# Kernel optimization log

Hardware: AMD Instinct MI355X
Metric: run time of the kernel (lower is better)

## Reference

```python
import jax, jax.numpy as jnp
import numpy as np


def setup_inputs() -> dict:
    key = jax.random.key(0)
    k1, k2 = jax.random.split(key)
    B, S, D = 8, 4096, 1024
    E, P = 8, 4
    x = jax.random.normal(k1, (B, S, D), dtype=jnp.float32)
    phi_kernel = jax.random.normal(k2, (D, E * P), dtype=jnp.float32) * (1.0 / np.sqrt(D))
    phi_bias = jnp.zeros((E * P,), dtype=jnp.float32)
    return {"x": x, "phi_kernel": phi_kernel, "phi_bias": phi_bias,
            "num_experts": E, "num_slots": P}


def reference(x, phi_kernel, phi_bias, num_experts, num_slots):
    B, S, D = x.shape
    E, P = num_experts, num_slots
    # phi logits: [B,S,E,P]
    phi_logits = (jnp.einsum('bsd,dk->bsk', x, phi_kernel) + phi_bias).reshape(B, S, E, P)
    # softmax over the sequence axis (each slot is a convex combo of tokens)
    phi_weights = jax.nn.softmax(phi_logits, axis=1)
    # soft slots: weighted sum over tokens -> [B,E,P,D] (fused, no [B,S,E,P,D] blowup)
    soft_slots = jnp.einsum('bsd,bsep->bepd', x, phi_weights)
    expert_inputs = soft_slots.reshape(B, E, P * D)
    expert_weights = jnp.full((B, S, E), 1.0 / E, dtype=x.dtype)
    expert_indices = jnp.broadcast_to(jnp.arange(E, dtype=jnp.int32)[None, None, :], (B, S, E))
    return (expert_weights, expert_indices, phi_weights, soft_slots, expert_inputs)
```

## Files before the change

kernel.cpp:

```cpp
#include <hip/hip_runtime.h>
#include <hip/hip_bf16.h>

#define B 8
#define S 4096
#define DD 1024
#define KK 32

typedef __attribute__((ext_vector_type(8))) short bf16x8;
typedef __attribute__((ext_vector_type(16))) float f32x16;
typedef __attribute__((ext_vector_type(4))) unsigned int u32x4;

static __device__ __forceinline__ unsigned short f2bf(float f) {
    unsigned int u = __builtin_bit_cast(unsigned int, f);
    u += 0x7FFFu + ((u >> 16) & 1u);
    return (unsigned short)(u >> 16);
}
static __device__ __forceinline__ unsigned int pkbf(float a, float b) {
    return (unsigned int)f2bf(a) | ((unsigned int)f2bf(b) << 16);
}
static __device__ __forceinline__ float bf2f(unsigned int u16) {
    return __builtin_bit_cast(float, u16 << 16);
}

__global__ __launch_bounds__(256) void k0_phit(const float* __restrict__ phi,
                                               unsigned short* __restrict__ phiT) {
    __shared__ float lt[32][33];
    const int d0 = blockIdx.x * 32;
    const int tid = threadIdx.x;
#pragma unroll
    for (int i = 0; i < 4; ++i) {
        int slot = tid + i * 256;
        int d = slot >> 5, k = slot & 31;
        lt[d][k] = phi[(size_t)(d0 + d) * KK + k];
    }
    __syncthreads();
    const int k = tid >> 3, c = tid & 7, d = c * 4;
    short4 pk;
    pk.x = (short)f2bf(lt[d + 0][k]);
    pk.y = (short)f2bf(lt[d + 1][k]);
    pk.z = (short)f2bf(lt[d + 2][k]);
    pk.w = (short)f2bf(lt[d + 3][k]);
    *(short4*)(phiT + (size_t)k * DD + d0 + d) = pk;
}

__global__ __launch_bounds__(256) void k1_logits(const float* __restrict__ x,
                                                 const unsigned short* __restrict__ phiT,
                                                 const float* __restrict__ bias,
                                                 unsigned short* __restrict__ lpb) {
    __shared__ float lt[4][32 * 33];

    const int tid = threadIdx.x;
    const int wv = __builtin_amdgcn_readfirstlane(tid >> 6);
    const int lane = tid & 63;
    const int l31 = lane & 31;
    const int half = lane >> 5;

    const int gw = blockIdx.x * 4 + wv;
    const int dq = gw & 3;
    const int stile = (gw >> 2) & 127;
    const int b = gw >> 9;
    const int s0 = stile * 32;

    const float* xr = x + ((size_t)(b * S + s0 + l31)) * DD + dq * 256 + half * 8;
    const unsigned short* pr = phiT + (size_t)l31 * DD + dq * 256 + half * 8;

    f32x16 acc;
    {
        float bv = (dq == 0) ? bias[l31] : 0.f;
#pragma unroll
        for (int r = 0; r < 16; ++r) acc[r] = bv;
    }

    float4 a0[2], a1[2];
    bf16x8 bf[2];
    auto ld = [&](int ks, int slot) {
        a0[slot] = *(const float4*)(xr + ks * 16);
        a1[slot] = *(const float4*)(xr + ks * 16 + 4);
        bf[slot] = *(const bf16x8*)(pr + ks * 16);
    };

    ld(0, 0);
    ld(1, 1);
#pragma unroll
    for (int ks = 0; ks < 16; ++ks) {
        const int cur = ks & 1;
        u32x4 t;
        t[0] = pkbf(a0[cur].x, a0[cur].y);
        t[1] = pkbf(a0[cur].z, a0[cur].w);
        t[2] = pkbf(a1[cur].x, a1[cur].y);
        t[3] = pkbf(a1[cur].z, a1[cur].w);
        bf16x8 af = __builtin_bit_cast(bf16x8, t);
        bf16x8 bc = bf[cur];
        if (ks < 14) ld(ks + 2, cur);
        acc = __builtin_amdgcn_mfma_f32_32x32x16_bf16(af, bc, acc, 0, 0, 0);
    }

    float* mylt = lt[wv];
#pragma unroll
    for (int r = 0; r < 16; ++r) {
        int row = (r & 3) + 8 * (r >> 2) + 4 * half;
        mylt[l31 * 33 + row] = acc[r];
    }
    {
        const int sb = half * 16;
        unsigned int w[8];
#pragma unroll
        for (int i = 0; i < 8; ++i)
            w[i] = pkbf(mylt[l31 * 33 + sb + 2 * i], mylt[l31 * 33 + sb + 2 * i + 1]);
        unsigned short* o = lpb + (((size_t)dq * B + b) * KK + l31) * S + s0 + sb;
        *(uint4*)o = make_uint4(w[0], w[1], w[2], w[3]);
        *(uint4*)(o + 8) = make_uint4(w[4], w[5], w[6], w[7]);
    }
}

__global__ __launch_bounds__(256) void k2_expsum(const unsigned short* __restrict__ lpb,
                                                 unsigned short* __restrict__ eT,
                                                 float* __restrict__ psum2) {
    const int bid = blockIdx.x;
    const int h = bid & 1;
    const int k = (bid >> 1) & 31;
    const int b = bid >> 6;
    const int tid = threadIdx.x;
    const int wave = tid >> 6, lane = tid & 63;

    const uint4* lp4 = (const uint4*)lpb;
    const size_t row4 = ((size_t)b * KK + k) * (S / 8) + h * 256 + tid;

    uint4 p0 = lp4[row4];
    uint4 p1 = lp4[(size_t)1 * (B * KK * S / 8) + row4];
    uint4 p2 = lp4[(size_t)2 * (B * KK * S / 8) + row4];
    uint4 p3 = lp4[(size_t)3 * (B * KK * S / 8) + row4];

    const unsigned int* q0 = &p0.x;
    const unsigned int* q1 = &p1.x;
    const unsigned int* q2 = &p2.x;
    const unsigned int* q3 = &p3.x;

    float e[8];
    float lsum = 0.f;
#pragma unroll
    for (int i = 0; i < 4; ++i) {
        float vlo = bf2f(q0[i] & 0xFFFFu) + bf2f(q1[i] & 0xFFFFu)
                  + bf2f(q2[i] & 0xFFFFu) + bf2f(q3[i] & 0xFFFFu);
        float vhi = bf2f(q0[i] >> 16) + bf2f(q1[i] >> 16)
                  + bf2f(q2[i] >> 16) + bf2f(q3[i] >> 16);
        e[2 * i] = __expf(vlo);
        e[2 * i + 1] = __expf(vhi);
        lsum += e[2 * i] + e[2 * i + 1];
    }
    uint4 o;
    o.x = pkbf(e[0], e[1]);
    o.y = pkbf(e[2], e[3]);
    o.z = pkbf(e[4], e[5]);
    o.w = pkbf(e[6], e[7]);
    ((uint4*)eT)[row4] = o;

#pragma unroll
    for (int off = 32; off >= 1; off >>= 1) lsum += __shfl_xor(lsum, off, 64);
    __shared__ float red[4];
    if (lane == 0) red[wave] = lsum;
    __syncthreads();
    if (tid == 0) psum2[(b * KK + k) * 2 + h] = red[0] + red[1] + red[2] + red[3];
}

__global__ __launch_bounds__(256) void k2b_linv(const float* __restrict__ psum2,
                                                float* __restrict__ Linv) {
    const int t = threadIdx.x;
    Linv[t] = 1.0f / (psum2[2 * t] + psum2[2 * t + 1]);
}

__global__ __launch_bounds__(256) void k2d_pw(const unsigned short* __restrict__ eT,
                                              const float* __restrict__ Linv,
                                              float* __restrict__ pw_out) {
    __shared__ float tile[128][33];
    const int b = blockIdx.x >> 5;
    const int sc = blockIdx.x & 31;
    const int s0 = sc * 128;
    const int tid = threadIdx.x;

    const int k = tid >> 3, part = tid & 7;
    const float scale = Linv[b * KK + k];
    const unsigned short* er = eT + ((size_t)b * KK + k) * S + s0 + part * 16;
    uint4 r0 = *(const uint4*)er;
    uint4 r1 = *(const uint4*)(er + 8);
    const unsigned int* q0 = &r0.x;
    const unsigned int* q1 = &r1.x;
#pragma unroll
    for (int i = 0; i < 4; ++i) {
        tile[part * 16 + 2 * i][k]     = bf2f(q0[i] & 0xFFFFu) * scale;
        tile[part * 16 + 2 * i + 1][k] = bf2f(q0[i] >> 16) * scale;
        tile[part * 16 + 8 + 2 * i][k]     = bf2f(q1[i] & 0xFFFFu) * scale;
        tile[part * 16 + 8 + 2 * i + 1][k] = bf2f(q1[i] >> 16) * scale;
    }
    __syncthreads();

    float* ob = pw_out + ((size_t)b * S + s0) * KK;
#pragma unroll
    for (int i = 0; i < 4; ++i) {
        const int idx4 = tid + i * 256;
        const int sl = idx4 >> 3, kq = idx4 & 7;
        float4 v4 = make_float4(tile[sl][kq * 4 + 0], tile[sl][kq * 4 + 1],
                                tile[sl][kq * 4 + 2], tile[sl][kq * 4 + 3]);
        ((float4*)ob)[idx4] = v4;
    }
}

__global__ __launch_bounds__(256) void k3_slots(const float* __restrict__ x,
                                                const unsigned short* __restrict__ eT,
                                                float* __restrict__ part) {
    const int tid = threadIdx.x;
    const int wv = __builtin_amdgcn_readfirstlane(tid >> 6);
    const int lane = tid & 63;
    const int l31 = lane & 31;
    const int half = lane >> 5;

    const int gw = blockIdx.x * 4 + wv;
    const int sc = gw & 7;
    const int dt = (gw >> 3) & 31;
    const int b = gw >> 8;

    const unsigned short* ar = eT + ((size_t)b * KK + l31) * S + sc * 512 + half * 8;
    const float* xc = x + ((size_t)(b * S + sc * 512 + half * 8)) * DD + dt * 32 + l31;

    f32x16 acc;
#pragma unroll
    for (int r = 0; r < 16; ++r) acc[r] = 0.f;

    float xb[2][8];
    bf16x8 ab[2];
    auto ld = [&](int ks, int slot) {
#pragma unroll
        for (int j = 0; j < 8; ++j)
            xb[slot][j] = xc[(size_t)(ks * 16 + j) * DD];
        ab[slot] = *(const bf16x8*)(ar + ks * 16);
    };

    ld(0, 0);
    ld(1, 1);
#pragma unroll 8
    for (int ks = 0; ks < 32; ++ks) {
        const int cur = ks & 1;
        u32x4 t;
        t[0] = pkbf(xb[cur][0], xb[cur][1]);
        t[1] = pkbf(xb[cur][2], xb[cur][3]);
        t[2] = pkbf(xb[cur][4], xb[cur][5]);
        t[3] = pkbf(xb[cur][6], xb[cur][7]);
        bf16x8 bfr = __builtin_bit_cast(bf16x8, t);
        bf16x8 ac = ab[cur];
        if (ks < 30) ld(ks + 2, cur);
        acc = __builtin_amdgcn_mfma_f32_32x32x16_bf16(ac, bfr, acc, 0, 0, 0);
    }

    float* pp = part + (((size_t)sc * B + b) * KK) * DD + dt * 32 + l31;
#pragma unroll
    for (int r = 0; r < 16; ++r) {
        int kmoe = (r & 3) + 8 * (r >> 2) + 4 * half;
        pp[(size_t)kmoe * DD] = acc[r];
    }
}

__global__ __launch_bounds__(256) void k4_finalize(const float* __restrict__ part,
                                                   const float* __restrict__ Linv,
                                                   float* __restrict__ out) {
    const int idx = blockIdx.x * 256 + threadIdx.x;
    const float4* p4 = (const float4*)part;

    float4 sv = p4[idx];
#pragma unroll
    for (int c = 1; c < 8; ++c) {
        float4 t = p4[(size_t)c * 65536 + idx];
        sv.x += t.x; sv.y += t.y; sv.z += t.z; sv.w += t.w;
    }
    const int f = idx * 4;
    const float scale = Linv[(f >> 15) * KK + ((f >> 10) & 31)];
    sv.x *= scale; sv.y *= scale; sv.z *= scale; sv.w *= scale;

    ((float4*)(out + 1572864))[idx] = sv;
    ((float4*)(out + 1835008))[idx] = sv;
    ((float4*)out)[idx] = make_float4(0.125f, 0.125f, 0.125f, 0.125f);
    float base = (float)(f & 7);
    ((float4*)(out + 262144))[idx] = make_float4(base, base + 1.f, base + 2.f, base + 3.f);
}

extern "C" void kernel_launch(void* const* d_in, const int* in_sizes, int n_in,
                              void* d_out, int out_size, void* d_ws, size_t ws_size,
                              hipStream_t stream) {
    const float* x    = (const float*)d_in[0];
    const float* phi  = (const float*)d_in[1];
    const float* bias = (const float*)d_in[2];
    float* out = (float*)d_out;

    float* ws = (float*)d_ws;
    unsigned short* lpb  = (unsigned short*)ws;
    unsigned short* eT   = (unsigned short*)(ws + 2097152);
    float* psum2 = ws + 2621440;
    float* Linv  = ws + 2621952;
    unsigned short* phiT = (unsigned short*)(ws + 2622208);
    float* part  = ws + 2638592;
    float* pw_out = out + 524288;

    k0_phit<<<dim3(32), dim3(256), 0, stream>>>(phi, phiT);
    k1_logits<<<dim3(1024), dim3(256), 0, stream>>>(x, phiT, bias, lpb);
    k2_expsum<<<dim3(512), dim3(256), 0, stream>>>(lpb, eT, psum2);
    k2b_linv<<<dim3(1), dim3(256), 0, stream>>>(psum2, Linv);
    k2d_pw<<<dim3(256), dim3(256), 0, stream>>>(eT, Linv, pw_out);
    k3_slots<<<dim3(512), dim3(256), 0, stream>>>(x, eT, part);
    k4_finalize<<<dim3(256), dim3(256), 0, stream>>>(part, Linv, out);
}
```

Baseline: 245.8 us.

## Fuse all stages into one cooperative persistent kernel with grid syncs

```diff
diff --git a/kernel.cpp b/kernel.cpp
--- a/kernel.cpp
+++ b/kernel.cpp
@@ -1,5 +1,8 @@
 #include <hip/hip_runtime.h>
 #include <hip/hip_bf16.h>
+#include <hip/hip_cooperative_groups.h>
+
+namespace cg = cooperative_groups;
 
 #define B 8
 #define S 4096
@@ -18,8 +21,223 @@
 static __device__ __forceinline__ unsigned int pkbf(float a, float b) {
     return (unsigned int)f2bf(a) | ((unsigned int)f2bf(b) << 16);
 }
+static __device__ __forceinline__ unsigned int pkbf_t(float lo, float hi) {
+    return __builtin_amdgcn_perm(__builtin_bit_cast(unsigned int, hi),
+                                 __builtin_bit_cast(unsigned int, lo),
+                                 0x07060302u);
+}
 static __device__ __forceinline__ float bf2f(unsigned int u16) {
     return __builtin_bit_cast(float, u16 << 16);
+}
+
+__global__ __launch_bounds__(256, 4) void fused_all(const float* __restrict__ x,
+                                                    const float* __restrict__ phi,
+                                                    const float* __restrict__ bias,
+                                                    float* __restrict__ ws,
+                                                    float* __restrict__ out) {
+    __shared__ __align__(16) char smraw[16896];
+    __shared__ float sLinv[256];
+    __shared__ float sred[4];
+
+    unsigned short* lpb = (unsigned short*)ws;
+    unsigned short* eT  = (unsigned short*)(ws + 2097152);
+    float* psum4 = ws + 2621440;
+    float* part  = ws + 2622464;
+    float* pw_out = out + 524288;
+
+    cg::grid_group grid = cg::this_grid();
+
+    const int bid = blockIdx.x;
+    const int tid = threadIdx.x;
+    const int wv = __builtin_amdgcn_readfirstlane(tid >> 6);
+    const int lane = tid & 63;
+    const int l31 = lane & 31;
+    const int half = lane >> 5;
+    const int nb = gridDim.x;
+
+    for (int gw = bid * 4 + wv; gw < 4096; gw += nb * 4) {
+        const int dq = gw & 3;
+        const int stile = (gw >> 2) & 127;
+        const int b = gw >> 9;
+        const int s0 = stile * 32;
+
+        const float* xr = x + ((size_t)(b * S + s0 + l31)) * DD + dq * 256 + half * 8;
+        const float* pcol = phi + (size_t)(dq * 256 + half * 8) * KK + l31;
+
+        f32x16 acc;
+        {
+            float bv = (dq == 0) ? bias[l31] : 0.f;
+#pragma unroll
+            for (int r = 0; r < 16; ++r) acc[r] = bv;
+        }
+
+        float4 a0[2], a1[2];
+        float pq[2][8];
+        auto ld = [&](int ks, int slot) {
+            a0[slot] = *(const float4*)(xr + ks * 16);
+            a1[slot] = *(const float4*)(xr + ks * 16 + 4);
+#pragma unroll
+            for (int j = 0; j < 8; ++j)
+                pq[slot][j] = pcol[(size_t)(ks * 16 + j) * KK];
+        };
+
+        ld(0, 0);
+        ld(1, 1);
+#pragma unroll
+        for (int ks = 0; ks < 16; ++ks) {
+            const int cur = ks & 1;
+            u32x4 ta, tb;
+            ta[0] = pkbf_t(a0[cur].x, a0[cur].y);
+            ta[1] = pkbf_t(a0[cur].z, a0[cur].w);
+            ta[2] = pkbf_t(a1[cur].x, a1[cur].y);
+            ta[3] = pkbf_t(a1[cur].z, a1[cur].w);
+            tb[0] = pkbf_t(pq[cur][0], pq[cur][1]);
+            tb[1] = pkbf_t(pq[cur][2], pq[cur][3]);
+            tb[2] = pkbf_t(pq[cur][4], pq[cur][5]);
+            tb[3] = pkbf_t(pq[cur][6], pq[cur][7]);
+            bf16x8 af = __builtin_bit_cast(bf16x8, ta);
+            bf16x8 bf = __builtin_bit_cast(bf16x8, tb);
+            if (ks < 14) ld(ks + 2, cur);
+            acc = __builtin_amdgcn_mfma_f32_32x32x16_bf16(af, bf, acc, 0, 0, 0);
+        }
+
+        float* mylt = (float*)smraw + wv * (32 * 33);
+#pragma unroll
+        for (int r = 0; r < 16; ++r) {
+            int row = (r & 3) + 8 * (r >> 2) + 4 * half;
+            mylt[l31 * 33 + row] = acc[r];
+        }
+        {
+            const int sb = half * 16;
+            unsigned int w[8];
+#pragma unroll
+            for (int i = 0; i < 8; ++i)
+                w[i] = pkbf_t(mylt[l31 * 33 + sb + 2 * i], mylt[l31 * 33 + sb + 2 * i + 1]);
+            unsigned short* o = lpb + (((size_t)dq * B + b) * KK + l31) * S + s0 + sb;
+            *(uint4*)o = make_uint4(w[0], w[1], w[2], w[3]);
+            *(uint4*)(o + 8) = make_uint4(w[4], w[5], w[6], w[7]);
+        }
+    }
+    grid.sync();
+
+    for (int u = bid; u < 1024; u += nb) {
+        const int q = u & 3;
+        const int k = (u >> 2) & 31;
+        const int b2 = u >> 7;
+        const unsigned int* base = (const unsigned int*)lpb;
+        const size_t row = ((size_t)(b2 * KK + k) * S + q * 1024) / 2 + tid * 2;
+
+        uint2 p0 = *(const uint2*)(base + row);
+        uint2 p1 = *(const uint2*)(base + 524288 + row);
+        uint2 p2 = *(const uint2*)(base + 2 * 524288 + row);
+        uint2 p3 = *(const uint2*)(base + 3 * 524288 + row);
+
+        float v0 = bf2f(p0.x & 0xFFFFu) + bf2f(p1.x & 0xFFFFu) + bf2f(p2.x & 0xFFFFu) + bf2f(p3.x & 0xFFFFu);
+        float v1 = bf2f(p0.x >> 16) + bf2f(p1.x >> 16) + bf2f(p2.x >> 16) + bf2f(p3.x >> 16);
+        float v2 = bf2f(p0.y & 0xFFFFu) + bf2f(p1.y & 0xFFFFu) + bf2f(p2.y & 0xFFFFu) + bf2f(p3.y & 0xFFFFu);
+        float v3 = bf2f(p0.y >> 16) + bf2f(p1.y >> 16) + bf2f(p2.y >> 16) + bf2f(p3.y >> 16);
+
+        float e0 = __expf(v0), e1 = __expf(v1), e2 = __expf(v2), e3 = __expf(v3);
+        float lsum = (e0 + e1) + (e2 + e3);
+
+        uint2 o;
+        o.x = pkbf_t(e0, e1);
+        o.y = pkbf_t(e2, e3);
+        *(uint2*)((unsigned int*)eT + row) = o;
+
+#pragma unroll
+        for (int off = 32; off >= 1; off >>= 1) lsum += __shfl_xor(lsum, off, 64);
+        if (lane == 0) sred[wv] = lsum;
+        __syncthreads();
+        if (tid == 0) psum4[(b2 * KK + k) * 4 + q] = sred[0] + sred[1] + sred[2] + sred[3];
+        __syncthreads();
+    }
+    grid.sync();
+
+    sLinv[tid & 255] = 1.0f / (psum4[(tid & 255) * 4] + psum4[(tid & 255) * 4 + 1] +
+                               psum4[(tid & 255) * 4 + 2] + psum4[(tid & 255) * 4 + 3]);
+    __syncthreads();
+
+    for (int gw = bid * 4 + wv; gw < 4096; gw += nb * 4) {
+        const int sc = gw & 15;
+        const int dt = (gw >> 4) & 31;
+        const int b2 = gw >> 9;
+
+        const unsigned short* ar = eT + ((size_t)b2 * KK + l31) * S + sc * 256 + half * 8;
+        const float* xc = x + ((size_t)(b2 * S + sc * 256 + half * 8)) * DD + dt * 32 + l31;
+
+        f32x16 acc;
+#pragma unroll
+        for (int r = 0; r < 16; ++r) acc[r] = 0.f;
+
+        float xb[2][8];
+        bf16x8 ab[2];
+        auto ld = [&](int ks, int slot) {
+#pragma unroll
+            for (int j = 0; j < 8; ++j)
+                xb[slot][j] = xc[(size_t)(ks * 16 + j) * DD];
+            ab[slot] = *(const bf16x8*)(ar + ks * 16);
+        };
+
+        ld(0, 0);
+        ld(1, 1);
+#pragma unroll
+        for (int ks = 0; ks < 16; ++ks) {
+            const int cur = ks & 1;
+            u32x4 t;
+            t[0] = pkbf_t(xb[cur][0], xb[cur][1]);
+            t[1] = pkbf_t(xb[cur][2], xb[cur][3]);
+            t[2] = pkbf_t(xb[cur][4], xb[cur][5]);
+            t[3] = pkbf_t(xb[cur][6], xb[cur][7]);
+            bf16x8 bfr = __builtin_bit_cast(bf16x8, t);
+            bf16x8 ac = ab[cur];
+            if (ks < 14) ld(ks + 2, cur);
+            acc = __builtin_amdgcn_mfma_f32_32x32x16_bf16(ac, bfr, acc, 0, 0, 0);
+        }
+
+        float* pp = part + (((size_t)sc * B + b2) * KK) * DD + dt * 32 + l31;
+#pragma unroll
+        for (int r = 0; r < 16; ++r) {
+            int kmoe = (r & 3) + 8 * (r >> 2) + 4 * half;
+            pp[(size_t)kmoe * DD] = acc[r];
+        }
+    }
+    __syncthreads();
+
+    for (int u = bid; u < 1024; u += nb) {
+        const int b2 = u >> 7;
+        const int sc = u & 127;
+        const int s0 = sc * 32;
+        float* tile = (float*)smraw;
+
+        const int k = tid >> 3, seg = tid & 7;
+        const float scale = sLinv[b2 * KK + k];
+        const unsigned int* er = (const unsigned int*)(eT + ((size_t)b2 * KK + k) * S + s0) + seg * 2;
+        uint2 r01 = *(const uint2*)er;
+        tile[(seg * 4 + 0) * 33 + k] = bf2f(r01.x & 0xFFFFu) * scale;
+        tile[(seg * 4 + 1) * 33 + k] = bf2f(r01.x >> 16) * scale;
+        tile[(seg * 4 + 2) * 33 + k] = bf2f(r01.y & 0xFFFFu) * scale;
+        tile[(seg * 4 + 3) * 33 + k] = bf2f(r01.y >> 16) * scale;
+        __syncthreads();
+
+        const int sl = tid >> 3, kq = tid & 7;
+        float4 v4 = make_float4(tile[sl * 33 + kq * 4 + 0], tile[sl * 33 + kq * 4 + 1],
+                                tile[sl * 33 + kq * 4 + 2], tile[sl * 33 + kq * 4 + 3]);
+        ((float4*)(pw_out + ((size_t)b2 * S + s0) * KK))[tid] = v4;
+        __syncthreads();
+    }
+    grid.sync();
+
+    for (int idx = bid * 256 + tid; idx < 262144; idx += nb * 256) {
+        float v = 0.f;
+#pragma unroll
+        for (int c = 0; c < 16; ++c) v += part[(size_t)c * 262144 + idx];
+        v *= sLinv[(idx >> 15) * KK + ((idx >> 10) & 31)];
+        out[1572864 + idx] = v;
+        out[1835008 + idx] = v;
+        out[idx] = 0.125f;
+        out[262144 + idx] = (float)(idx & 7);
+    }
 }
 
 __global__ __launch_bounds__(256) void k0_phit(const float* __restrict__ phi,
@@ -48,13 +266,11 @@
                                                  const float* __restrict__ bias,
                                                  unsigned short* __restrict__ lpb) {
     __shared__ float lt[4][32 * 33];
-
     const int tid = threadIdx.x;
     const int wv = __builtin_amdgcn_readfirstlane(tid >> 6);
     const int lane = tid & 63;
     const int l31 = lane & 31;
     const int half = lane >> 5;
-
     const int gw = blockIdx.x * 4 + wv;
     const int dq = gw & 3;
     const int stile = (gw >> 2) & 127;
@@ -70,7 +286,6 @@
 #pragma unroll
         for (int r = 0; r < 16; ++r) acc[r] = bv;
     }
-
     float4 a0[2], a1[2];
     bf16x8 bf[2];
     auto ld = [&](int ks, int slot) {
@@ -78,7 +293,6 @@
         a1[slot] = *(const float4*)(xr + ks * 16 + 4);
         bf[slot] = *(const bf16x8*)(pr + ks * 16);
     };
-
     ld(0, 0);
     ld(1, 1);
 #pragma unroll
@@ -94,7 +308,6 @@
         if (ks < 14) ld(ks + 2, cur);
         acc = __builtin_amdgcn_mfma_f32_32x32x16_bf16(af, bc, acc, 0, 0, 0);
     }
-
     float* mylt = lt[wv];
 #pragma unroll
     for (int r = 0; r < 16; ++r) {
@@ -122,20 +335,16 @@
     const int b = bid >> 6;
     const int tid = threadIdx.x;
     const int wave = tid >> 6, lane = tid & 63;
-
     const uint4* lp4 = (const uint4*)lpb;
     const size_t row4 = ((size_t)b * KK + k) * (S / 8) + h * 256 + tid;
-
     uint4 p0 = lp4[row4];
     uint4 p1 = lp4[(size_t)1 * (B * KK * S / 8) + row4];
     uint4 p2 = lp4[(size_t)2 * (B * KK * S / 8) + row4];
     uint4 p3 = lp4[(size_t)3 * (B * KK * S / 8) + row4];
-
     const unsigned int* q0 = &p0.x;
     const unsigned int* q1 = &p1.x;
     const unsigned int* q2 = &p2.x;
     const unsigned int* q3 = &p3.x;
-
     float e[8];
     float lsum = 0.f;
 #pragma unroll
@@ -154,7 +363,6 @@
     o.z = pkbf(e[4], e[5]);
     o.w = pkbf(e[6], e[7]);
     ((uint4*)eT)[row4] = o;
-
 #pragma unroll
     for (int off = 32; off >= 1; off >>= 1) lsum += __shfl_xor(lsum, off, 64);
     __shared__ float red[4];
@@ -177,7 +385,6 @@
     const int sc = blockIdx.x & 31;
     const int s0 = sc * 128;
     const int tid = threadIdx.x;
-
     const int k = tid >> 3, part = tid & 7;
     const float scale = Linv[b * KK + k];
     const unsigned short* er = eT + ((size_t)b * KK + k) * S + s0 + part * 16;
@@ -193,7 +400,6 @@
         tile[part * 16 + 8 + 2 * i + 1][k] = bf2f(q1[i] >> 16) * scale;
     }
     __syncthreads();
-
     float* ob = pw_out + ((size_t)b * S + s0) * KK;
 #pragma unroll
     for (int i = 0; i < 4; ++i) {
@@ -213,19 +419,15 @@
     const int lane = tid & 63;
     const int l31 = lane & 31;
     const int half = lane >> 5;
-
     const int gw = blockIdx.x * 4 + wv;
     const int sc = gw & 7;
     const int dt = (gw >> 3) & 31;
     const int b = gw >> 8;
-
     const unsigned short* ar = eT + ((size_t)b * KK + l31) * S + sc * 512 + half * 8;
     const float* xc = x + ((size_t)(b * S + sc * 512 + half * 8)) * DD + dt * 32 + l31;
-
     f32x16 acc;
 #pragma unroll
     for (int r = 0; r < 16; ++r) acc[r] = 0.f;
-
     float xb[2][8];
     bf16x8 ab[2];
     auto ld = [&](int ks, int slot) {
@@ -234,7 +436,6 @@
             xb[slot][j] = xc[(size_t)(ks * 16 + j) * DD];
         ab[slot] = *(const bf16x8*)(ar + ks * 16);
     };
-
     ld(0, 0);
     ld(1, 1);
 #pragma unroll 8
@@ -250,7 +451,6 @@
         if (ks < 30) ld(ks + 2, cur);
         acc = __builtin_amdgcn_mfma_f32_32x32x16_bf16(ac, bfr, acc, 0, 0, 0);
     }
-
     float* pp = part + (((size_t)sc * B + b) * KK) * DD + dt * 32 + l31;
 #pragma unroll
     for (int r = 0; r < 16; ++r) {
@@ -264,7 +464,6 @@
                                                    float* __restrict__ out) {
     const int idx = blockIdx.x * 256 + threadIdx.x;
     const float4* p4 = (const float4*)part;
-
     float4 sv = p4[idx];
 #pragma unroll
     for (int c = 1; c < 8; ++c) {
@@ -274,7 +473,6 @@
     const int f = idx * 4;
     const float scale = Linv[(f >> 15) * KK + ((f >> 10) & 31)];
     sv.x *= scale; sv.y *= scale; sv.z *= scale; sv.w *= scale;
-
     ((float4*)(out + 1572864))[idx] = sv;
     ((float4*)(out + 1835008))[idx] = sv;
     ((float4*)out)[idx] = make_float4(0.125f, 0.125f, 0.125f, 0.125f);
@@ -289,21 +487,32 @@
     const float* phi  = (const float*)d_in[1];
     const float* bias = (const float*)d_in[2];
     float* out = (float*)d_out;
-
     float* ws = (float*)d_ws;
-    unsigned short* lpb  = (unsigned short*)ws;
-    unsigned short* eT   = (unsigned short*)(ws + 2097152);
-    float* psum2 = ws + 2621440;
-    float* Linv  = ws + 2621952;
-    unsigned short* phiT = (unsigned short*)(ws + 2622208);
-    float* part  = ws + 2638592;
-    float* pw_out = out + 524288;
-
-    k0_phit<<<dim3(32), dim3(256), 0, stream>>>(phi, phiT);
-    k1_logits<<<dim3(1024), dim3(256), 0, stream>>>(x, phiT, bias, lpb);
-    k2_expsum<<<dim3(512), dim3(256), 0, stream>>>(lpb, eT, psum2);
-    k2b_linv<<<dim3(1), dim3(256), 0, stream>>>(psum2, Linv);
-    k2d_pw<<<dim3(256), dim3(256), 0, stream>>>(eT, Linv, pw_out);
-    k3_slots<<<dim3(512), dim3(256), 0, stream>>>(x, eT, part);
-    k4_finalize<<<dim3(256), dim3(256), 0, stream>>>(part, Linv, out);
-}
+
+    void* args[] = {(void*)&x, (void*)&phi, (void*)&bias, (void*)&ws, (void*)&out};
+    hipError_t err = hipLaunchCooperativeKernel((const void*)fused_all, dim3(1024),
+                                                dim3(256), args, 0, stream);
+    if (err != hipSuccess) {
+        (void)hipGetLastError();
+        err = hipLaunchCooperativeKernel((const void*)fused_all, dim3(512),
+                                         dim3(256), args, 0, stream);
+    }
+    if (err != hipSuccess) {
+        (void)hipGetLastError();
+        unsigned short* lpb  = (unsigned short*)ws;
+        unsigned short* eT   = (unsigned short*)(ws + 2097152);
+        float* psum2 = ws + 2621440;
+        float* Linv  = ws + 2621952;
+        unsigned short* phiT = (unsigned short*)(ws + 2622208);
+        float* part  = ws + 2638592;
+        float* pw_out = out + 524288;
+
+        k0_phit<<<dim3(32), dim3(256), 0, stream>>>(phi, phiT);
+        k1_logits<<<dim3(1024), dim3(256), 0, stream>>>(x, phiT, bias, lpb);
+        k2_expsum<<<dim3(512), dim3(256), 0, stream>>>(lpb, eT, psum2);
+        k2b_linv<<<dim3(1), dim3(256), 0, stream>>>(psum2, Linv);
+        k2d_pw<<<dim3(256), dim3(256), 0, stream>>>(eT, Linv, pw_out);
+        k3_slots<<<dim3(512), dim3(256), 0, stream>>>(x, eT, part);
+        k4_finalize<<<dim3(256), dim3(256), 0, stream>>>(part, Linv, out);
+    }
+}
```

Result: slower. 634.0 us (+158.0%).
